# Performance work log

Hardware: AMD Instinct MI355X
Metric: run time of the kernel (lower is better)

## Reference

```python
import jax, jax.numpy as jnp
import numpy as np
from math import sqrt

DIM = 64
N_HEADS = 12
B, T = 4, 2048


def setup_inputs() -> dict:
    key = jax.random.key(0)
    ks = jax.random.split(key, 5)
    scale = 1.0 / sqrt(DIM)
    x = jax.random.normal(ks[0], (B, T, DIM), dtype=jnp.float32)
    # torch Linear(dim, h*dim) weight is (h*dim, dim); store transposed (dim, h*dim)
    Wq = jax.random.uniform(ks[1], (DIM, N_HEADS * DIM), dtype=jnp.float32, minval=-scale, maxval=scale)
    Wk = jax.random.uniform(ks[2], (DIM, N_HEADS * DIM), dtype=jnp.float32, minval=-scale, maxval=scale)
    Wv = jax.random.uniform(ks[3], (DIM, N_HEADS * DIM), dtype=jnp.float32, minval=-scale, maxval=scale)
    # finalDense: Linear(h*dim, dim) -> stored (h*dim, dim)
    Wo = jax.random.uniform(ks[4], (N_HEADS * DIM, DIM), dtype=jnp.float32,
                            minval=-1.0 / sqrt(N_HEADS * DIM), maxval=1.0 / sqrt(N_HEADS * DIM))
    return {"x": x, "Wq": Wq, "Wk": Wk, "Wv": Wv, "Wo": Wo}


def reference(x, Wq, Wk, Wv, Wo):
    b, t, k = x.shape
    h = Wq.shape[1] // k
    # NOTE: the original module does .view(b,t,h,k).view(b*h,t,k), a flat
    # row-major memory reinterpretation (NOT a head transpose). jnp.reshape
    # is the same flat reshape, so this is faithful.
    Q = (x @ Wq).reshape(b * h, t, k)
    K = (x @ Wk).reshape(b * h, t, k)
    V = (x @ Wv).reshape(b * h, t, k)
    # W[b,i,j] = sum_k K[b,i,k] * Q[b,j,k], scaled; softmax over j (last dim)
    W = jnp.einsum('bik,bjk->bij', K, Q) / sqrt(k)
    W = jax.nn.softmax(W, axis=2)
    Z = jnp.einsum('bij,bjk->bik', W, V)  # (b*h, t, k)
    Z = Z.reshape(b, t, h * k)  # flat reinterpretation, matches torch views
    return Z @ Wo
```

## Files before the change

### kernel.cpp

```cpp
#include <hip/hip_runtime.h>
#include <hip/hip_bf16.h>


#define DIM 64
#define NH 12
#define HD 768
#define BT 8192
#define TSEQ 2048
#define NSLICE 48
#define SLICE (TSEQ*DIM)

#define LDQ 72
#define LDT 72

#define SWZ(r, c) ((r) * LDQ + (((((c) >> 3) - 2 * (r)) & 7) << 3) + ((c) & 7))

typedef unsigned short ushort;
typedef __attribute__((ext_vector_type(8))) short bf16x8;
typedef __attribute__((ext_vector_type(4))) short bf16x4;
typedef __attribute__((ext_vector_type(4))) float f32x4;
typedef __attribute__((ext_vector_type(16))) float f32x16;
typedef __attribute__((ext_vector_type(4))) unsigned int uint32x4;

#define SCALE2 0.18033688011112042f

__device__ __forceinline__ ushort f2b(float f) {
    union { float f; unsigned int i; } v; v.f = f;
    unsigned int x = v.i;
    return (ushort)((x + 0x7fffu + ((x >> 16) & 1u)) >> 16);
}

__global__ __launch_bounds__(256) void prep_w(
    const float* __restrict__ Wq, const float* __restrict__ Wk,
    const float* __restrict__ Wv, const float* __restrict__ Wo,
    ushort* __restrict__ Wt, ushort* __restrict__ Wot)
{
    __shared__ float tile[64][65];
    int bx = blockIdx.x;
    int z = bx / 12, bt = bx % 12;
    const float* __restrict__ IN = (z == 0) ? Wq : (z == 1) ? Wk : (z == 2) ? Wv : Wo;
    int inStride  = (z < 3) ? HD : DIM;
    int outStride = (z < 3) ? DIM : HD;
    int rbase = (z < 3) ? 0 : bt * 64;
    int cbase = (z < 3) ? bt * 64 : 0;
    ushort* __restrict__ OUT = (z < 3) ? (Wt + (size_t)z * HD * DIM) : Wot;
    int t = threadIdx.x;
    int r = t >> 2, c0 = (t & 3) * 16;
    #pragma unroll
    for (int cc = 0; cc < 16; cc += 4) {
        float4 a = *(const float4*)&IN[(size_t)(rbase + r) * inStride + cbase + c0 + cc];
        tile[r][c0 + cc] = a.x; tile[r][c0 + cc + 1] = a.y;
        tile[r][c0 + cc + 2] = a.z; tile[r][c0 + cc + 3] = a.w;
    }
    __syncthreads();
    int cl = t >> 2, r0 = (t & 3) * 16;
    ushort tmp[16] __attribute__((aligned(16)));
    #pragma unroll
    for (int rr = 0; rr < 16; ++rr) tmp[rr] = f2b(tile[r0 + rr][cl]);
    *(float4*)&OUT[(size_t)(cbase + cl) * outStride + rbase + r0] = *(const float4*)tmp;
    *(float4*)&OUT[(size_t)(cbase + cl) * outStride + rbase + r0 + 8] = *(const float4*)&tmp[8];
}

__global__ __launch_bounds__(256) void qkv_kernel(
    const float* __restrict__ x, const ushort* __restrict__ Wt,
    ushort* __restrict__ Q, ushort* __restrict__ K, ushort* __restrict__ V)
{
    int rt = blockIdx.x, yg = blockIdx.y;
    int t = threadIdx.x, w = t >> 6, lane = t & 63;
    int ln = lane & 15, q = lane >> 4;
    int m0 = rt * 64 + w * 16;

    float4 xa = *(const float4*)&x[(size_t)(m0 + ln) * DIM + q * 8];
    float4 xb_ = *(const float4*)&x[(size_t)(m0 + ln) * DIM + q * 8 + 4];
    float4 xc = *(const float4*)&x[(size_t)(m0 + ln) * DIM + 32 + q * 8];
    float4 xd = *(const float4*)&x[(size_t)(m0 + ln) * DIM + 32 + q * 8 + 4];
    ushort ta[8] __attribute__((aligned(16)));
    ushort tb[8] __attribute__((aligned(16)));
    ta[0]=f2b(xa.x); ta[1]=f2b(xa.y); ta[2]=f2b(xa.z); ta[3]=f2b(xa.w);
    ta[4]=f2b(xb_.x); ta[5]=f2b(xb_.y); ta[6]=f2b(xb_.z); ta[7]=f2b(xb_.w);
    tb[0]=f2b(xc.x); tb[1]=f2b(xc.y); tb[2]=f2b(xc.z); tb[3]=f2b(xc.w);
    tb[4]=f2b(xd.x); tb[5]=f2b(xd.y); tb[6]=f2b(xd.z); tb[7]=f2b(xd.w);
    bf16x8 af0 = *(const bf16x8*)ta;
    bf16x8 af1 = *(const bf16x8*)tb;

    for (int cc = 0; cc < 6; ++cc) {
        int ct = yg * 6 + cc;
        int which = ct / 12;
        int col0 = (ct % 12) * 64;
        const ushort* __restrict__ Wz = Wt + (size_t)which * HD * DIM;
        ushort* __restrict__ Y = (which == 0) ? Q : (which == 1) ? K : V;
        float sc = (which == 0) ? SCALE2 : 1.f;
        #pragma unroll
        for (int nt = 0; nt < 4; ++nt) {
            int n = col0 + nt * 16 + ln;
            bf16x8 bf0 = *(const bf16x8*)&Wz[(size_t)n * DIM + q * 8];
            bf16x8 bf1 = *(const bf16x8*)&Wz[(size_t)n * DIM + 32 + q * 8];
            f32x4 acc = (f32x4){0.f, 0.f, 0.f, 0.f};
            acc = __builtin_amdgcn_mfma_f32_16x16x32_bf16(af0, bf0, acc, 0, 0, 0);
            acc = __builtin_amdgcn_mfma_f32_16x16x32_bf16(af1, bf1, acc, 0, 0, 0);
            #pragma unroll
            for (int r = 0; r < 4; ++r)
                Y[(size_t)(m0 + q * 4 + r) * HD + col0 + nt * 16 + ln] = f2b(acc[r] * sc);
        }
    }
}

__global__ __launch_bounds__(256) void vtrans_kernel(
    const ushort* __restrict__ V, ushort* __restrict__ Vt)
{
    __shared__ ushort tileT[64 * LDT];
    int tt = blockIdx.x, s = blockIdx.y;
    const ushort* __restrict__ Vp = V + (size_t)s * SLICE;
    ushort* __restrict__ Vo = Vt + (size_t)s * SLICE;
    int t = threadIdx.x;
    int r = t >> 3, c = (t & 7) * 8;
    ushort va[8] __attribute__((aligned(16)));
    ushort vb[8] __attribute__((aligned(16)));
    *(float4*)va = *(const float4*)&Vp[(size_t)(tt * 64 + r) * DIM + c];
    *(float4*)vb = *(const float4*)&Vp[(size_t)(tt * 64 + r + 32) * DIM + c];
    int g0 = ((r >> 3) ^ (c >> 3)) * 8 + (r & 7);
    int g1 = (((r + 32) >> 3) ^ (c >> 3)) * 8 + (r & 7);
    #pragma unroll
    for (int k = 0; k < 8; ++k) {
        tileT[(c + k) * LDT + g0] = va[k];
        tileT[(c + k) * LDT + g1] = vb[k];
    }
    __syncthreads();
    #pragma unroll
    for (int j = 0; j < 2; ++j) {
        int flat = t + 256 * j;
        int d = flat >> 3, tg = flat & 7;
        int sg = tg ^ ((d >> 3) & 7);
        float4 vv = *(const float4*)&tileT[d * LDT + sg * 8];
        *(float4*)&Vo[(size_t)d * TSEQ + tt * 64 + tg * 8] = vv;
    }
}

__global__ __launch_bounds__(256, 3) void attn_kernel(
    const ushort* __restrict__ Qs, const ushort* __restrict__ Ks,
    const ushort* __restrict__ Vts, ushort* __restrict__ Zs)
{
    __shared__ ushort sh[4 * 64 * LDQ];
    int itile = blockIdx.x, s = blockIdx.y;
    const ushort* __restrict__ Qp = Qs + (size_t)s * SLICE;
    const ushort* __restrict__ Kp = Ks + (size_t)s * SLICE;
    const ushort* __restrict__ Vp = Vts + (size_t)s * SLICE;
    ushort* __restrict__ Zp = Zs + (size_t)s * SLICE;
    int t = threadIdx.x, w = t >> 6, lane = t & 63;
    int i5 = lane & 31, hi = lane >> 5;

    bf16x8 kf[4];
    {
        size_t krow = (size_t)(itile * 128 + w * 32 + i5) * DIM;
        #pragma unroll
        for (int c = 0; c < 4; ++c)
            kf[c] = *(const bf16x8*)&Kp[krow + c * 16 + hi * 8];
    }

    f32x16 Of0, Of1;
    #pragma unroll
    for (int r = 0; r < 16; ++r) { Of0[r] = 0.f; Of1[r] = 0.f; }
    float lsum = 0.f;

    int sr = t >> 3, sc = (t & 7) * 8;
    const ushort* qsrc0 = &Qp[(size_t)sr * DIM + sc];
    const ushort* qsrc1 = &Qp[(size_t)(sr + 32) * DIM + sc];
    const ushort* vsrc0 = &Vp[(size_t)sr * TSEQ + sc];
    const ushort* vsrc1 = &Vp[(size_t)(sr + 32) * TSEQ + sc];

    float4 qa0 = *(const float4*)qsrc0;
    float4 qa1 = *(const float4*)qsrc1;
    float4 va0 = *(const float4*)vsrc0;
    float4 va1 = *(const float4*)vsrc1;
    {
        ushort* Q0 = sh;
        ushort* V0 = sh + 2 * 64 * LDQ;
        *(float4*)&Q0[SWZ(sr, sc)] = qa0;
        *(float4*)&Q0[SWZ(sr + 32, sc)] = qa1;
        *(float4*)&V0[SWZ(sr, sc)] = va0;
        *(float4*)&V0[SWZ(sr + 32, sc)] = va1;
    }
    qa0 = *(const float4*)(qsrc0 + 64 * DIM);
    qa1 = *(const float4*)(qsrc1 + 64 * DIM);
    va0 = *(const float4*)(vsrc0 + 64);
    va1 = *(const float4*)(vsrc1 + 64);
    __syncthreads();

    for (int tt = 0; tt < 32; ++tt) {
        int ib = tt & 1;
        const ushort* Qc = sh + ib * (64 * LDQ);
        const ushort* Vc = sh + (2 + ib) * (64 * LDQ);
        if (tt < 31) {
            ushort* Qn = sh + (ib ^ 1) * (64 * LDQ);
            ushort* Vn = sh + (2 + (ib ^ 1)) * (64 * LDQ);
            *(float4*)&Qn[SWZ(sr, sc)] = qa0;
            *(float4*)&Qn[SWZ(sr + 32, sc)] = qa1;
            *(float4*)&Vn[SWZ(sr, sc)] = va0;
            *(float4*)&Vn[SWZ(sr + 32, sc)] = va1;
            if (tt < 30) {
                size_t qo = (size_t)(tt + 2) * 64 * DIM;
                int vo = (tt + 2) * 64;
                qa0 = *(const float4*)(qsrc0 + qo);
                qa1 = *(const float4*)(qsrc1 + qo);
                va0 = *(const float4*)(vsrc0 + vo);
                va1 = *(const float4*)(vsrc1 + vo);
            }
        }
        #pragma unroll
        for (int js = 0; js < 2; ++js) {
            f32x16 acc;
            #pragma unroll
            for (int r = 0; r < 16; ++r) acc[r] = 0.f;
            #pragma unroll
            for (int c = 0; c < 4; ++c) {
                bf16x8 aQ = *(const bf16x8*)&Qc[SWZ(js * 32 + i5, c * 16 + hi * 8)];
                acc = __builtin_amdgcn_mfma_f32_32x32x16_bf16(aQ, kf[c], acc, 0, 0, 0);
            }
            unsigned wv[8];
            float ls = 0.f;
            #pragma unroll
            for (int k = 0; k < 8; ++k) {
                float p0 = __builtin_amdgcn_exp2f(acc[2 * k]);
                float p1 = __builtin_amdgcn_exp2f(acc[2 * k + 1]);
                unsigned int b0 = __float_as_uint(p0), b1 = __float_as_uint(p1);
                unsigned int t1 = b1 & 0xFFFF0000u;
                unsigned int h = (b0 >> 16) | t1;
                ls += __uint_as_float(h << 16) + __uint_as_float(t1);
                wv[k] = h;
            }
            lsum += ls;
            uint32x4 u0 = { wv[0], wv[1], wv[2], wv[3] };
            uint32x4 u1 = { wv[4], wv[5], wv[6], wv[7] };
            bf16x8 pa0 = __builtin_bit_cast(bf16x8, u0);
            bf16x8 pa1 = __builtin_bit_cast(bf16x8, u1);
            #pragma unroll
            for (int dt = 0; dt < 2; ++dt) {
                int vr = dt * 32 + i5;
                int uc = js * 32 + 4 * hi;
                bf16x4 v0a = *(const bf16x4*)&Vc[SWZ(vr, uc)];
                bf16x4 v0b = *(const bf16x4*)&Vc[SWZ(vr, uc + 8)];
                bf16x4 v1a = *(const bf16x4*)&Vc[SWZ(vr, uc + 16)];
                bf16x4 v1b = *(const bf16x4*)&Vc[SWZ(vr, uc + 24)];
                bf16x8 vb0 = __builtin_shufflevector(v0a, v0b, 0, 1, 2, 3, 4, 5, 6, 7);
                bf16x8 vb1 = __builtin_shufflevector(v1a, v1b, 0, 1, 2, 3, 4, 5, 6, 7);
                if (dt == 0) {
                    Of0 = __builtin_amdgcn_mfma_f32_32x32x16_bf16(pa0, vb0, Of0, 0, 0, 0);
                    Of0 = __builtin_amdgcn_mfma_f32_32x32x16_bf16(pa1, vb1, Of0, 0, 0, 0);
                } else {
                    Of1 = __builtin_amdgcn_mfma_f32_32x32x16_bf16(pa0, vb0, Of1, 0, 0, 0);
                    Of1 = __builtin_amdgcn_mfma_f32_32x32x16_bf16(pa1, vb1, Of1, 0, 0, 0);
                }
            }
        }
        __syncthreads();
    }

    float l = lsum + __shfl_xor(lsum, 32);
    float linv = 1.f / l;
    #pragma unroll
    for (int r = 0; r < 16; ++r) {
        int cr = (r & 3) + 8 * (r >> 2);
        float li = __shfl(linv, cr + 4 * hi);
        int row = w * 32 + cr + 4 * hi;
        sh[SWZ(row, i5)]      = f2b(Of0[r] * li);
        sh[SWZ(row, 32 + i5)] = f2b(Of1[r] * li);
    }
    __syncthreads();
    int zr = t >> 1, zc = (t & 1) * 32;
    size_t zoff = (size_t)(itile * 128 + zr) * DIM + zc;
    #pragma unroll
    for (int c4 = 0; c4 < 4; ++c4)
        *(float4*)&Zp[zoff + c4 * 8] = *(const float4*)&sh[SWZ(zr, zc + c4 * 8)];
}

__global__ __launch_bounds__(256) void out_kernel(
    const ushort* __restrict__ Z, const ushort* __restrict__ Wot,
    float* __restrict__ out)
{
    int t = threadIdx.x, w = t >> 6, lane = t & 63;
    int m0 = blockIdx.x * 64 + w * 16;
    int ln = lane & 15, q = lane >> 4;
    f32x4 acc[4];
    #pragma unroll
    for (int nt = 0; nt < 4; ++nt) acc[nt] = (f32x4){0.f, 0.f, 0.f, 0.f};
    for (int kc = 0; kc < 24; ++kc) {
        bf16x8 a = *(const bf16x8*)&Z[(size_t)(m0 + ln) * HD + kc * 32 + q * 8];
        #pragma unroll
        for (int nt = 0; nt < 4; ++nt) {
            bf16x8 bf = *(const bf16x8*)&Wot[(size_t)(nt * 16 + ln) * HD + kc * 32 + q * 8];
            acc[nt] = __builtin_amdgcn_mfma_f32_16x16x32_bf16(a, bf, acc[nt], 0, 0, 0);
        }
    }
    #pragma unroll
    for (int nt = 0; nt < 4; ++nt)
        #pragma unroll
        for (int r = 0; r < 4; ++r)
            out[(size_t)(m0 + q * 4 + r) * DIM + nt * 16 + ln] = acc[nt][r];
}

extern "C" void kernel_launch(void* const* d_in, const int* in_sizes, int n_in,
                              void* d_out, int out_size, void* d_ws, size_t ws_size,
                              hipStream_t stream)
{
    const float* x  = (const float*)d_in[0];
    const float* Wq = (const float*)d_in[1];
    const float* Wk = (const float*)d_in[2];
    const float* Wv = (const float*)d_in[3];
    const float* Wo = (const float*)d_in[4];
    float* out = (float*)d_out;

    const size_t n = (size_t)BT * HD;
    ushort* Q   = (ushort*)d_ws;
    ushort* K   = Q + n;
    ushort* V   = K + n;
    ushort* Vt  = V + n;
    ushort* Wt  = Vt;
    ushort* Wot = Vt + n;
    ushort* Z   = V;

    prep_w<<<48, 256, 0, stream>>>(Wq, Wk, Wv, Wo, Wt, Wot);
    qkv_kernel<<<dim3(128, 6), 256, 0, stream>>>(x, Wt, Q, K, V);
    vtrans_kernel<<<dim3(32, 48), 256, 0, stream>>>(V, Vt);
    attn_kernel<<<dim3(16, 48), 256, 0, stream>>>(Q, K, Vt, Z);
    out_kernel<<<128, 256, 0, stream>>>(Z, Wot, out);
}
```

Measured before the change: 179.9 us.

## Use two-wave attention blocks with 64 rows per wave and unswizzled LDS

The attention kernel moves from 4 waves of 32 K-rows each to 2 waves of 64 K-rows each. Each Q fragment read from LDS now feeds two MFMA row-halves and each V fragment feeds two output accumulators, which halves LDS reads per unit of MFMA work. The XOR-style swizzle on LDS indexing is dropped in favour of plain padded row-major addressing. The cost is higher register pressure from four output accumulators and doubled K fragments, fewer waves per block for latency hiding, and a possible rise in LDS bank conflicts now that the swizzle is gone.

```diff
diff --git a/kernel.cpp b/kernel.cpp
--- a/kernel.cpp
+++ b/kernel.cpp
@@ -12,8 +12,6 @@
 
 #define LDQ 72
 #define LDT 72
-
-#define SWZ(r, c) ((r) * LDQ + (((((c) >> 3) - 2 * (r)) & 7) << 3) + ((c) & 7))
 
 typedef unsigned short ushort;
 typedef __attribute__((ext_vector_type(8))) short bf16x8;
@@ -136,7 +134,7 @@
     }
 }
 
-__global__ __launch_bounds__(256, 3) void attn_kernel(
+__global__ __launch_bounds__(128, 2) void attn_kernel(
     const ushort* __restrict__ Qs, const ushort* __restrict__ Ks,
     const ushort* __restrict__ Vts, ushort* __restrict__ Zs)
 {
@@ -149,41 +147,45 @@
     int t = threadIdx.x, w = t >> 6, lane = t & 63;
     int i5 = lane & 31, hi = lane >> 5;
 
-    bf16x8 kf[4];
-    {
-        size_t krow = (size_t)(itile * 128 + w * 32 + i5) * DIM;
+    bf16x8 kf[2][4];
+    #pragma unroll
+    for (int ih = 0; ih < 2; ++ih) {
+        size_t krow = (size_t)(itile * 128 + w * 64 + ih * 32 + i5) * DIM;
         #pragma unroll
         for (int c = 0; c < 4; ++c)
-            kf[c] = *(const bf16x8*)&Kp[krow + c * 16 + hi * 8];
-    }
-
-    f32x16 Of0, Of1;
-    #pragma unroll
-    for (int r = 0; r < 16; ++r) { Of0[r] = 0.f; Of1[r] = 0.f; }
-    float lsum = 0.f;
+            kf[ih][c] = *(const bf16x8*)&Kp[krow + c * 16 + hi * 8];
+    }
+
+    f32x16 Of[2][2];
+    #pragma unroll
+    for (int ih = 0; ih < 2; ++ih)
+        #pragma unroll
+        for (int dt = 0; dt < 2; ++dt)
+            #pragma unroll
+            for (int r = 0; r < 16; ++r) Of[ih][dt][r] = 0.f;
+    float lsum[2] = {0.f, 0.f};
 
     int sr = t >> 3, sc = (t & 7) * 8;
-    const ushort* qsrc0 = &Qp[(size_t)sr * DIM + sc];
-    const ushort* qsrc1 = &Qp[(size_t)(sr + 32) * DIM + sc];
-    const ushort* vsrc0 = &Vp[(size_t)sr * TSEQ + sc];
-    const ushort* vsrc1 = &Vp[(size_t)(sr + 32) * TSEQ + sc];
-
-    float4 qa0 = *(const float4*)qsrc0;
-    float4 qa1 = *(const float4*)qsrc1;
-    float4 va0 = *(const float4*)vsrc0;
-    float4 va1 = *(const float4*)vsrc1;
+    float4 qa[4], va[4];
+    #pragma unroll
+    for (int k = 0; k < 4; ++k) {
+        qa[k] = *(const float4*)&Qp[(size_t)(sr + 16 * k) * DIM + sc];
+        va[k] = *(const float4*)&Vp[(size_t)(sr + 16 * k) * TSEQ + sc];
+    }
     {
         ushort* Q0 = sh;
         ushort* V0 = sh + 2 * 64 * LDQ;
-        *(float4*)&Q0[SWZ(sr, sc)] = qa0;
-        *(float4*)&Q0[SWZ(sr + 32, sc)] = qa1;
-        *(float4*)&V0[SWZ(sr, sc)] = va0;
-        *(float4*)&V0[SWZ(sr + 32, sc)] = va1;
-    }
-    qa0 = *(const float4*)(qsrc0 + 64 * DIM);
-    qa1 = *(const float4*)(qsrc1 + 64 * DIM);
-    va0 = *(const float4*)(vsrc0 + 64);
-    va1 = *(const float4*)(vsrc1 + 64);
+        #pragma unroll
+        for (int k = 0; k < 4; ++k) {
+            *(float4*)&Q0[(sr + 16 * k) * LDQ + sc] = qa[k];
+            *(float4*)&V0[(sr + 16 * k) * LDQ + sc] = va[k];
+        }
+    }
+    #pragma unroll
+    for (int k = 0; k < 4; ++k) {
+        qa[k] = *(const float4*)&Qp[(size_t)(64 + sr + 16 * k) * DIM + sc];
+        va[k] = *(const float4*)&Vp[(size_t)(sr + 16 * k) * TSEQ + 64 + sc];
+    }
     __syncthreads();
 
     for (int tt = 0; tt < 32; ++tt) {
@@ -193,84 +195,98 @@
         if (tt < 31) {
             ushort* Qn = sh + (ib ^ 1) * (64 * LDQ);
             ushort* Vn = sh + (2 + (ib ^ 1)) * (64 * LDQ);
-            *(float4*)&Qn[SWZ(sr, sc)] = qa0;
-            *(float4*)&Qn[SWZ(sr + 32, sc)] = qa1;
-            *(float4*)&Vn[SWZ(sr, sc)] = va0;
-            *(float4*)&Vn[SWZ(sr + 32, sc)] = va1;
+            #pragma unroll
+            for (int k = 0; k < 4; ++k) {
+                *(float4*)&Qn[(sr + 16 * k) * LDQ + sc] = qa[k];
+                *(float4*)&Vn[(sr + 16 * k) * LDQ + sc] = va[k];
+            }
             if (tt < 30) {
                 size_t qo = (size_t)(tt + 2) * 64 * DIM;
                 int vo = (tt + 2) * 64;
-                qa0 = *(const float4*)(qsrc0 + qo);
-                qa1 = *(const float4*)(qsrc1 + qo);
-                va0 = *(const float4*)(vsrc0 + vo);
-                va1 = *(const float4*)(vsrc1 + vo);
+                #pragma unroll
+                for (int k = 0; k < 4; ++k) {
+                    qa[k] = *(const float4*)&Qp[(size_t)(sr + 16 * k) * DIM + qo + sc];
+                    va[k] = *(const float4*)&Vp[(size_t)(sr + 16 * k) * TSEQ + vo + sc];
+                }
             }
         }
         #pragma unroll
         for (int js = 0; js < 2; ++js) {
-            f32x16 acc;
-            #pragma unroll
-            for (int r = 0; r < 16; ++r) acc[r] = 0.f;
-            #pragma unroll
-            for (int c = 0; c < 4; ++c) {
-                bf16x8 aQ = *(const bf16x8*)&Qc[SWZ(js * 32 + i5, c * 16 + hi * 8)];
-                acc = __builtin_amdgcn_mfma_f32_32x32x16_bf16(aQ, kf[c], acc, 0, 0, 0);
-            }
-            unsigned wv[8];
-            float ls = 0.f;
-            #pragma unroll
-            for (int k = 0; k < 8; ++k) {
-                float p0 = __builtin_amdgcn_exp2f(acc[2 * k]);
-                float p1 = __builtin_amdgcn_exp2f(acc[2 * k + 1]);
-                unsigned int b0 = __float_as_uint(p0), b1 = __float_as_uint(p1);
-                unsigned int t1 = b1 & 0xFFFF0000u;
-                unsigned int h = (b0 >> 16) | t1;
-                ls += __uint_as_float(h << 16) + __uint_as_float(t1);
-                wv[k] = h;
-            }
-            lsum += ls;
-            uint32x4 u0 = { wv[0], wv[1], wv[2], wv[3] };
-            uint32x4 u1 = { wv[4], wv[5], wv[6], wv[7] };
-            bf16x8 pa0 = __builtin_bit_cast(bf16x8, u0);
-            bf16x8 pa1 = __builtin_bit_cast(bf16x8, u1);
+            bf16x8 aQ[4];
+            #pragma unroll
+            for (int c = 0; c < 4; ++c)
+                aQ[c] = *(const bf16x8*)&Qc[(js * 32 + i5) * LDQ + c * 16 + hi * 8];
+            f32x16 acc[2];
+            #pragma unroll
+            for (int ih = 0; ih < 2; ++ih) {
+                #pragma unroll
+                for (int r = 0; r < 16; ++r) acc[ih][r] = 0.f;
+                #pragma unroll
+                for (int c = 0; c < 4; ++c)
+                    acc[ih] = __builtin_amdgcn_mfma_f32_32x32x16_bf16(aQ[c], kf[ih][c], acc[ih], 0, 0, 0);
+            }
+            bf16x8 pa[2][2];
+            #pragma unroll
+            for (int ih = 0; ih < 2; ++ih) {
+                unsigned wv[8];
+                float ls = 0.f;
+                #pragma unroll
+                for (int k = 0; k < 8; ++k) {
+                    float p0 = __builtin_amdgcn_exp2f(acc[ih][2 * k]);
+                    float p1 = __builtin_amdgcn_exp2f(acc[ih][2 * k + 1]);
+                    unsigned int b0 = __float_as_uint(p0), b1 = __float_as_uint(p1);
+                    unsigned int t1 = b1 & 0xFFFF0000u;
+                    unsigned int h = (b0 >> 16) | t1;
+                    ls += __uint_as_float(h << 16) + __uint_as_float(t1);
+                    wv[k] = h;
+                }
+                lsum[ih] += ls;
+                uint32x4 u0 = { wv[0], wv[1], wv[2], wv[3] };
+                uint32x4 u1 = { wv[4], wv[5], wv[6], wv[7] };
+                pa[ih][0] = __builtin_bit_cast(bf16x8, u0);
+                pa[ih][1] = __builtin_bit_cast(bf16x8, u1);
+            }
             #pragma unroll
             for (int dt = 0; dt < 2; ++dt) {
-                int vr = dt * 32 + i5;
-                int uc = js * 32 + 4 * hi;
-                bf16x4 v0a = *(const bf16x4*)&Vc[SWZ(vr, uc)];
-                bf16x4 v0b = *(const bf16x4*)&Vc[SWZ(vr, uc + 8)];
-                bf16x4 v1a = *(const bf16x4*)&Vc[SWZ(vr, uc + 16)];
-                bf16x4 v1b = *(const bf16x4*)&Vc[SWZ(vr, uc + 24)];
+                int vbase = (dt * 32 + i5) * LDQ + js * 32 + 4 * hi;
+                bf16x4 v0a = *(const bf16x4*)&Vc[vbase];
+                bf16x4 v0b = *(const bf16x4*)&Vc[vbase + 8];
+                bf16x4 v1a = *(const bf16x4*)&Vc[vbase + 16];
+                bf16x4 v1b = *(const bf16x4*)&Vc[vbase + 24];
                 bf16x8 vb0 = __builtin_shufflevector(v0a, v0b, 0, 1, 2, 3, 4, 5, 6, 7);
                 bf16x8 vb1 = __builtin_shufflevector(v1a, v1b, 0, 1, 2, 3, 4, 5, 6, 7);
-                if (dt == 0) {
-                    Of0 = __builtin_amdgcn_mfma_f32_32x32x16_bf16(pa0, vb0, Of0, 0, 0, 0);
-                    Of0 = __builtin_amdgcn_mfma_f32_32x32x16_bf16(pa1, vb1, Of0, 0, 0, 0);
-                } else {
-                    Of1 = __builtin_amdgcn_mfma_f32_32x32x16_bf16(pa0, vb0, Of1, 0, 0, 0);
-                    Of1 = __builtin_amdgcn_mfma_f32_32x32x16_bf16(pa1, vb1, Of1, 0, 0, 0);
+                #pragma unroll
+                for (int ih = 0; ih < 2; ++ih) {
+                    Of[ih][dt] = __builtin_amdgcn_mfma_f32_32x32x16_bf16(pa[ih][0], vb0, Of[ih][dt], 0, 0, 0);
+                    Of[ih][dt] = __builtin_amdgcn_mfma_f32_32x32x16_bf16(pa[ih][1], vb1, Of[ih][dt], 0, 0, 0);
                 }
             }
         }
         __syncthreads();
     }
 
-    float l = lsum + __shfl_xor(lsum, 32);
-    float linv = 1.f / l;
-    #pragma unroll
-    for (int r = 0; r < 16; ++r) {
-        int cr = (r & 3) + 8 * (r >> 2);
-        float li = __shfl(linv, cr + 4 * hi);
-        int row = w * 32 + cr + 4 * hi;
-        sh[SWZ(row, i5)]      = f2b(Of0[r] * li);
-        sh[SWZ(row, 32 + i5)] = f2b(Of1[r] * li);
+    #pragma unroll
+    for (int ih = 0; ih < 2; ++ih) {
+        float l = lsum[ih] + __shfl_xor(lsum[ih], 32);
+        float linv = 1.f / l;
+        #pragma unroll
+        for (int r = 0; r < 16; ++r) {
+            int cr = (r & 3) + 8 * (r >> 2);
+            float li = __shfl(linv, cr + 4 * hi);
+            int row = w * 64 + ih * 32 + cr + 4 * hi;
+            sh[row * LDQ + i5]      = f2b(Of[ih][0][r] * li);
+            sh[row * LDQ + 32 + i5] = f2b(Of[ih][1][r] * li);
+        }
     }
     __syncthreads();
-    int zr = t >> 1, zc = (t & 1) * 32;
-    size_t zoff = (size_t)(itile * 128 + zr) * DIM + zc;
-    #pragma unroll
-    for (int c4 = 0; c4 < 4; ++c4)
-        *(float4*)&Zp[zoff + c4 * 8] = *(const float4*)&sh[SWZ(zr, zc + c4 * 8)];
+    #pragma unroll
+    for (int p = 0; p < 2; ++p) {
+        int zr = p * 64 + (t >> 1), zc = (t & 1) * 32;
+        size_t zoff = (size_t)(itile * 128 + zr) * DIM + zc;
+        #pragma unroll
+        for (int c4 = 0; c4 < 4; ++c4)
+            *(float4*)&Zp[zoff + c4 * 8] = *(const float4*)&sh[zr * LDQ + zc + c4 * 8];
+    }
 }
 
 __global__ __launch_bounds__(256) void out_kernel(
@@ -321,6 +337,6 @@
     prep_w<<<48, 256, 0, stream>>>(Wq, Wk, Wv, Wo, Wt, Wot);
     qkv_kernel<<<dim3(128, 6), 256, 0, stream>>>(x, Wt, Q, K, V);
     vtrans_kernel<<<dim3(32, 48), 256, 0, stream>>>(V, Vt);
-    attn_kernel<<<dim3(16, 48), 256, 0, stream>>>(Q, K, Vt, Z);
+    attn_kernel<<<dim3(16, 48), 128, 0, stream>>>(Q, K, Vt, Z);
     out_kernel<<<128, 256, 0, stream>>>(Z, Wot, out);
 }
```

Measured after the change: 228.7 us. +27.1%, slower.
